# Kernel optimization log

Measured on AMD Instinct MI355X. Metric: run time of the kernel, lower is better.

## Reference

```python
import jax, jax.numpy as jnp
import numpy as np

B, T, C, H = 2, 2048, 1024, 16
N = C // H
MISS_ROWS = 128


def _rwkv7_scan(q, w_log, k, v, a, b):
    # all [B,T,H,N] float32 (bf16-rounded). RWKV7 delta-rule recurrence:
    #   S_t = S_{t-1} * diag(exp(w_t)) + (S_{t-1} a_t) b_t^T + v_t k_t^T
    #   o_t = S_t q_t   (state S has shape [B,H,Nv,Nk]; decay along k-dim)
    Bq, Tq, Hq, Nq = q.shape

    def step(S, inp):
        q_t, w_t, k_t, v_t, a_t, b_t = inp
        ew = jnp.exp(w_t)  # decay in (0,1) since w_log = -exp(...) < 0
        sa = jnp.einsum('bhvi,bhi->bhv', S, a_t)
        S = S * ew[:, :, None, :] + sa[..., None] * b_t[:, :, None, :] + v_t[..., None] * k_t[:, :, None, :]
        o = jnp.einsum('bhvj,bhj->bhv', S, q_t)
        return S, o

    xs = tuple(jnp.moveaxis(u, 1, 0) for u in (q, w_log, k, v, a, b))
    S0 = jnp.zeros((Bq, Hq, Nq, Nq), jnp.float32)
    _, o = jax.lax.scan(step, S0, xs)
    return jnp.moveaxis(o, 0, 1)  # [B,T,H,N]


def setup_inputs() -> dict:
    key = jax.random.key(0)
    ks = jax.random.split(key, 16)
    f32 = jnp.float32
    return {
        'residual': jax.random.normal(ks[0], (B, T, C), f32),
        'x': jax.random.normal(ks[1], (B, T, C), f32),
        'x0': jax.random.normal(ks[2], (B, T, C), f32),
        'dx0': jax.random.normal(ks[3], (B, T, C), f32),
        'Wq': jax.random.normal(ks[4], (C, C), f32) * 0.02,
        'Wk': jax.random.normal(ks[5], (C, C), f32) * 0.02,
        'Wv': jax.random.normal(ks[6], (C, C), f32) * 0.02,
        'Wproj': jax.random.normal(ks[7], (C, C), f32) * 0.02,
        'x_q': jax.random.uniform(ks[8], (1, 1, C), f32),
        'x_k': jax.random.uniform(ks[9], (1, 1, C), f32),
        'x_v': jax.random.uniform(ks[10], (1, 1, C), f32),
        'v0': 0.7 + 0.1 * jax.random.normal(ks[11], (1, 1, C), f32),
        'w0': -3.0 + 0.5 * jax.random.normal(ks[12], (1, 1, C), f32),
        'a0': 0.1 * jax.random.normal(ks[13], (1, 1, C), f32),
        'miss': jax.random.normal(ks[14], (MISS_ROWS, 4 * C), f32) * 0.02,
        'r_k': 0.1 * jax.random.normal(ks[15], (H, N), f32),
    }


def reference(residual, x, x0, dx0, Wq, Wk, Wv, Wproj, x_q, x_k, x_v, v0, w0, a0, miss, r_k):
    Bx, Tx, Cx = x.shape
    Hh, Nn = r_k.shape
    # token shift: dx_prev = x_{t-1} - x_t (zero-padded at t=0)
    dx_prev = jnp.concatenate([jnp.zeros_like(x[:, :1]), x[:, :-1]], axis=1) - x
    q = (x + dx_prev * x_q) @ Wq.T
    k = (x + dx_prev * x_k) @ Wk.T
    v = (x + dx_prev * x_v) @ Wv.T
    deltas = x[:, :, :miss.shape[0]] @ miss  # [B,T,4C]
    w_delta, v_delta, a_delta, g = jnp.split(deltas, 4, axis=-1)
    log_neglog_w = -jax.nn.softplus(-(w0 + w_delta)) - 0.5
    log_w = -jnp.exp(log_neglog_w)  # log decay, always < 0
    v_first = (x0 + dx0 * x_v) @ Wv.T
    v = v + (v_first - v) * jax.nn.sigmoid(v0 + v_delta)
    g = 1.0 + g
    a = jax.nn.sigmoid(a0 + a_delta)
    kh = k.reshape(Bx, Tx, Hh, Nn)
    kk = kh / jnp.maximum(jnp.linalg.norm(kh, axis=-1, keepdims=True), 1e-12)
    kk = kk.reshape(Bx, Tx, Cx)
    k = k * a
    z = -kk
    b = kk * a
    bf = lambda u: u.astype(jnp.bfloat16).astype(jnp.float32).reshape(Bx, Tx, Hh, Nn)
    qh, wh, kh2, vh, zh, bh = (bf(u) for u in (q, log_w, k, v, z, b))
    y = _rwkv7_scan(qh, wh, kh2, vh, zh, bh) * (float(Nn) ** -0.5)  # [B,T,H,N]
    xnorm = jnp.linalg.norm(x.reshape(Bx, Tx, Hh, Nn), axis=-1, keepdims=True)
    vnorm = jnp.linalg.norm(vh, axis=-1, keepdims=True)
    u = (1.0 - xnorm / (vnorm + 1e-12)) * jax.nn.sigmoid(r_k)
    y = (y + vh * u).reshape(Bx, Tx, Cx)
    y = y * g
    return residual + y @ Wproj.T
```

## Files before the change

### kernel.cpp

```cpp
#include <hip/hip_runtime.h>
#include <stdint.h>
#include <stddef.h>

#define B_ 2
#define T_ 2048
#define C_ 1024
#define H_ 16
#define N_ 64
#define M_ (B_*T_)
#define L_ 128
#define NC_ (T_/L_)

typedef unsigned short ushort_t;
typedef __attribute__((ext_vector_type(8))) __bf16 bf16x8;
typedef __attribute__((ext_vector_type(4))) float  f32x4;

__device__ __forceinline__ ushort_t f2bf(float x){
  uint32_t u = __float_as_uint(x);
  u += 0x7fffu + ((u >> 16) & 1u);
  return (ushort_t)(u >> 16);
}
__device__ __forceinline__ float bf2f(uint32_t hu){
  return __uint_as_float(hu << 16);
}
__device__ __forceinline__ void ldbf16x16(const ushort_t* p, float* o){
  uint4 u0 = *(const uint4*)p;
  uint4 u1 = *(const uint4*)(p+8);
  o[0]=bf2f(u0.x&0xffffu); o[1]=bf2f(u0.x>>16);
  o[2]=bf2f(u0.y&0xffffu); o[3]=bf2f(u0.y>>16);
  o[4]=bf2f(u0.z&0xffffu); o[5]=bf2f(u0.z>>16);
  o[6]=bf2f(u0.w&0xffffu); o[7]=bf2f(u0.w>>16);
  o[8]=bf2f(u1.x&0xffffu); o[9]=bf2f(u1.x>>16);
  o[10]=bf2f(u1.y&0xffffu); o[11]=bf2f(u1.y>>16);
  o[12]=bf2f(u1.z&0xffffu); o[13]=bf2f(u1.z>>16);
  o[14]=bf2f(u1.w&0xffffu); o[15]=bf2f(u1.w>>16);
}

__device__ __forceinline__ ushort4 mixq4(float4 a, float4 p, float4 c){
  ushort4 o;
  o.x = f2bf(fmaf(p.x - a.x, c.x, a.x));
  o.y = f2bf(fmaf(p.y - a.y, c.y, a.y));
  o.z = f2bf(fmaf(p.z - a.z, c.z, a.z));
  o.w = f2bf(fmaf(p.w - a.w, c.w, a.w));
  return o;
}
__global__ __launch_bounds__(256) void prep_all(
    const float* __restrict__ x, const float* __restrict__ x0,
    const float* __restrict__ dx0,
    const float* __restrict__ xq, const float* __restrict__ xk,
    const float* __restrict__ xv,
    const float* __restrict__ Wq, const float* __restrict__ Wk,
    const float* __restrict__ Wv, const float* __restrict__ Wp,
    const float* __restrict__ miss,
    ushort_t* __restrict__ Aq, ushort_t* __restrict__ Ak,
    ushort_t* __restrict__ Av, ushort_t* __restrict__ Axf,
    ushort_t* __restrict__ Xb,
    ushort_t* __restrict__ Wb, ushort_t* __restrict__ Wpb,
    ushort_t* __restrict__ missT)
{
  __shared__ ushort_t tile[128][66];
  const int blk = blockIdx.x;
  const int tid = threadIdx.x;
  if (blk < 4096){
    const int idx = blk*256 + tid;
    const int col4 = idx & 255;
    const int i = idx >> 8;
    const int t = i & (T_-1);
    float4 a = ((const float4*)x)[idx];
    float4 p = {0.f,0.f,0.f,0.f};
    if (t > 0) p = ((const float4*)x)[idx - 256];
    float4 cq = ((const float4*)xq)[col4];
    float4 ck = ((const float4*)xk)[col4];
    float4 cv = ((const float4*)xv)[col4];
    ((ushort4*)Aq)[idx] = mixq4(a, p, cq);
    ((ushort4*)Ak)[idx] = mixq4(a, p, ck);
    ((ushort4*)Av)[idx] = mixq4(a, p, cv);
    float4 z = ((const float4*)x0)[idx];
    float4 d = ((const float4*)dx0)[idx];
    ushort4 of;
    of.x = f2bf(fmaf(d.x, cv.x, z.x));
    of.y = f2bf(fmaf(d.y, cv.y, z.y));
    of.z = f2bf(fmaf(d.z, cv.z, z.z));
    of.w = f2bf(fmaf(d.w, cv.w, z.w));
    ((ushort4*)Axf)[idx] = of;
    ushort4 ob = {f2bf(a.x), f2bf(a.y), f2bf(a.z), f2bf(a.w)};
    ((ushort4*)Xb)[idx] = ob;
  } else if (blk < 4096 + 5*1024){
    const int y = (blk - 4096) >> 10;
    const float* src = (y==0)?Wq:(y==1)?Wk:(y<4)?Wv:Wp;
    ushort_t* dst = (y<4) ? Wb + (size_t)y*C_*C_ : Wpb;
    const int idx = ((blk - 4096) & 1023)*256 + tid;
    float4 v = ((const float4*)src)[idx];
    ushort4 o = {f2bf(v.x), f2bf(v.y), f2bf(v.z), f2bf(v.w)};
    ((ushort4*)dst)[idx] = o;
  } else {
    const int j0 = (blk - 4096 - 5*1024)*64;
#pragma unroll
    for (int rep=0; rep<8; rep++){
      int k = rep*16 + (tid>>4);
      int jj = (tid&15)*4;
      float4 v = *(const float4*)&miss[(size_t)k*4096 + j0 + jj];
      tile[k][jj+0]=f2bf(v.x); tile[k][jj+1]=f2bf(v.y);
      tile[k][jj+2]=f2bf(v.z); tile[k][jj+3]=f2bf(v.w);
    }
    __syncthreads();
#pragma unroll
    for (int rep=0; rep<8; rep++){
      int j = tid>>2;
      int kk = (tid&3)*32 + rep*4;
      ushort4 o = {tile[kk+0][j], tile[kk+1][j], tile[kk+2][j], tile[kk+3][j]};
      *(ushort4*)&missT[(size_t)(j0+j)*128 + kk] = o;
    }
  }
}

__global__ __launch_bounds__(256, 2) void mfma_gemm(
    const ushort_t* __restrict__ Ab, int lda, int64_t Asz,
    const ushort_t* __restrict__ Bbp, int ldb, int64_t Bsz,
    void* __restrict__ Cb, int ldc, int64_t Csz, int c_bf16,
    const float* __restrict__ resid, int K)
{
  const ushort_t* A  = Ab  + (size_t)blockIdx.z * Asz;
  const ushort_t* Bm = Bbp + (size_t)blockIdx.z * Bsz;
  const int i0 = blockIdx.y * 128;
  const int j0 = blockIdx.x * 128;
  const int tid = threadIdx.x;
  const int lane = tid & 63;
  const int w = tid >> 6;
  const int wm = w & 1, wn = w >> 1;

  __shared__ ushort_t As[128*32];
  __shared__ ushort_t Bs[128*32];

  f32x4 acc[4][4];
#pragma unroll
  for (int i=0;i<4;i++)
#pragma unroll
    for (int j=0;j<4;j++) acc[i][j] = (f32x4){0.f,0.f,0.f,0.f};

  const int lr = lane >> 2;
  const int ls = lane & 3;
  const ushort_t* ga = A  + (size_t)(i0 + w*32 + lr)*lda + ls*8;
  const ushort_t* gb = Bm + (size_t)(j0 + w*32 + lr)*ldb + ls*8;
  const int lm = lane & 15, lq = lane >> 4;

  for (int k0 = 0; k0 < K; k0 += 32){
    __syncthreads();
#pragma unroll
    for (int p=0;p<2;p++){
      __builtin_amdgcn_global_load_lds(
        (const __attribute__((address_space(1))) void*)(ga + (size_t)p*16*lda + k0),
        (__attribute__((address_space(3))) void*)&As[(w*32 + p*16)*32], 16, 0, 0);
      __builtin_amdgcn_global_load_lds(
        (const __attribute__((address_space(1))) void*)(gb + (size_t)p*16*ldb + k0),
        (__attribute__((address_space(3))) void*)&Bs[(w*32 + p*16)*32], 16, 0, 0);
    }
    __syncthreads();
    bf16x8 af[4], bfr[4];
#pragma unroll
    for (int i=0;i<4;i++)
      af[i] = *(const bf16x8*)&As[(wm*64 + i*16 + lm)*32 + lq*8];
#pragma unroll
    for (int j=0;j<4;j++)
      bfr[j] = *(const bf16x8*)&Bs[(wn*64 + j*16 + lm)*32 + lq*8];
#pragma unroll
    for (int i=0;i<4;i++)
#pragma unroll
      for (int j=0;j<4;j++)
        acc[i][j] = __builtin_amdgcn_mfma_f32_16x16x32_bf16(af[i], bfr[j], acc[i][j], 0, 0, 0);
  }

  if (!c_bf16){
    float* C = (float*)Cb + (size_t)blockIdx.z * Csz;
#pragma unroll
    for (int i=0;i<4;i++)
#pragma unroll
      for (int j=0;j<4;j++)
#pragma unroll
        for (int r=0;r<4;r++){
          const int row = i0 + wm*64 + i*16 + lq*4 + r;
          const int col = j0 + wn*64 + j*16 + lm;
          float v = acc[i][j][r];
          if (resid) v += resid[(size_t)row*ldc + col];
          C[(size_t)row*ldc + col] = v;
        }
  } else {
    ushort_t* C = (ushort_t*)Cb + (size_t)blockIdx.z * Csz;
#pragma unroll
    for (int i=0;i<4;i++)
#pragma unroll
      for (int j=0;j<4;j++)
#pragma unroll
        for (int r=0;r<4;r++){
          const int row = i0 + wm*64 + i*16 + lq*4 + r;
          const int col = j0 + wn*64 + j*16 + lm;
          C[(size_t)row*ldc + col] = f2bf(acc[i][j][r]);
        }
  }
}

__global__ __launch_bounds__(256) void fuse_kernel(
    const float* __restrict__ qm, const float* __restrict__ km,
    const float* __restrict__ vm, const float* __restrict__ vfm,
    const ushort_t* __restrict__ del, const float* __restrict__ x,
    const float* __restrict__ w0, const float* __restrict__ v0,
    const float* __restrict__ a0,
    uint32_t* __restrict__ packed, float* __restrict__ gout,
    float* __restrict__ ratio)
{
  const int lane = threadIdx.x & 63;
  const int ht = blockIdx.x*4 + (threadIdx.x >> 6);
  const int i = ht >> 4;
  const int h = ht & 15;
  const int c = h*64 + lane;
  const size_t ic = (size_t)i*C_ + c;
  float qv = qm[ic], kv = km[ic], vv = vm[ic], vfv = vfm[ic], xv = x[ic];
  const size_t d0 = (size_t)i*4*C_ + c;
  float wd = bf2f(del[d0]), vd = bf2f(del[d0+C_]);
  float ad = bf2f(del[d0+2*C_]), gd = bf2f(del[d0+3*C_]);

  float z1 = -(w0[c]+wd);
  float sp = fmaxf(z1, 0.f) + log1pf(expf(-fabsf(z1)));
  float logw = -expf(-sp - 0.5f);
  float sv = 1.f/(1.f+expf(-(v0[c]+vd)));
  vv = vv + (vfv - vv)*sv;
  float gv = 1.f + gd;
  float av = 1.f/(1.f+expf(-(a0[c]+ad)));

  ushort_t vr_u = f2bf(vv);
  float vrf = bf2f(vr_u);

  float ksq = kv*kv, xsq = xv*xv, vsq = vrf*vrf;
#pragma unroll
  for (int off=32; off>0; off>>=1){
    ksq += __shfl_xor(ksq, off, 64);
    xsq += __shfl_xor(xsq, off, 64);
    vsq += __shfl_xor(vsq, off, 64);
  }
  float kn = sqrtf(ksq);
  float kkn = kv / fmaxf(kn, 1e-12f);
  float k2 = kv*av;
  float zv = -kkn;
  float bv = kkn*av;

  uint32_t p0 = (uint32_t)f2bf(logw) | ((uint32_t)f2bf(zv) << 16);
  uint32_t p1 = (uint32_t)f2bf(bv)   | ((uint32_t)f2bf(k2) << 16);
  uint32_t p2 = (uint32_t)f2bf(qv)   | ((uint32_t)vr_u << 16);
  uint32_t* pb = packed + ((size_t)ht*64 + lane)*3;
  pb[0]=p0; pb[1]=p1; pb[2]=p2;
  gout[ic] = gv;
  if (lane == 0)
    ratio[ht] = 1.f - sqrtf(xsq)/(sqrtf(vsq)+1e-12f);
}


__global__ __launch_bounds__(256) void chunk_mdp_kernel(
    const uint32_t* __restrict__ packed,
    float* __restrict__ phi, float* __restrict__ cc, float* __restrict__ md)
{
  const int blk = blockIdx.x;
  const int c  = blk & (NC_-1);
  const int bh = blk >> 4;
  const int b = bh >> 4, h = bh & 15;
  const int tid = threadIdx.x;
  const int rp = tid >> 2;
  const int qr = tid & 3;
  const int t0 = c * L_;

  __shared__ float    ewS[4][N_], vS[4][N_];
  __shared__ ushort_t zS[4][N_], bS[4][N_], qS[4][N_], kS[4][N_];

  float X[16], Z[16];
#pragma unroll
  for (int i=0;i<16;i++){ X[i] = (qr*16+i == rp) ? 1.f : 0.f; Z[i] = 0.f; }

  const int s = tid >> 6, d = tid & 63;
  size_t ap = (((size_t)(b*T_+t0+s))*H_ + h)*64 + d;
  uint32_t pu0 = packed[ap*3], pu1 = packed[ap*3+1], pu2 = packed[ap*3+2];

  for (int tg = 0; tg < L_; tg += 4){
    __syncthreads();
    ewS[s][d] = __expf(bf2f(pu0 & 0xffffu));
    zS[s][d]  = (ushort_t)(pu0 >> 16);
    bS[s][d]  = (ushort_t)(pu1 & 0xffffu);
    kS[s][d]  = (ushort_t)(pu1 >> 16);
    qS[s][d]  = (ushort_t)(pu2 & 0xffffu);
    vS[s][d]  = bf2f(pu2 >> 16);
    if (tg + 4 < L_){
      size_t a2 = (((size_t)(b*T_+t0+tg+4+s))*H_ + h)*64 + d;
      pu0 = packed[a2*3]; pu1 = packed[a2*3+1]; pu2 = packed[a2*3+2];
    }
    __syncthreads();
#pragma unroll 1
    for (int ss=0; ss<4; ss++){
      float zf[16], ef[16], bf[16], qf[16], kf[16];
      ldbf16x16(&zS[ss][qr*16], zf);
      ldbf16x16(&bS[ss][qr*16], bf);
      ldbf16x16(&qS[ss][qr*16], qf);
      ldbf16x16(&kS[ss][qr*16], kf);
#pragma unroll
      for (int i4=0;i4<4;i4++)
        *(float4*)&ef[i4*4] = *(const float4*)&ewS[ss][qr*16+i4*4];
      const float vr = vS[ss][rp];
      float a0=0.f,a1=0.f,a2=0.f,a3=0.f, c0=0.f,c1=0.f,c2=0.f,c3=0.f;
#pragma unroll
      for (int i=0;i<16;i+=4){
        a0 = fmaf(X[i+0], zf[i+0], a0); a1 = fmaf(X[i+1], zf[i+1], a1);
        a2 = fmaf(X[i+2], zf[i+2], a2); a3 = fmaf(X[i+3], zf[i+3], a3);
        c0 = fmaf(Z[i+0], zf[i+0], c0); c1 = fmaf(Z[i+1], zf[i+1], c1);
        c2 = fmaf(Z[i+2], zf[i+2], c2); c3 = fmaf(Z[i+3], zf[i+3], c3);
      }
      float sx = (a0+a1)+(a2+a3);
      float sz = (c0+c1)+(c2+c3);
      sx += __shfl_xor(sx,1,64); sx += __shfl_xor(sx,2,64);
      sz += __shfl_xor(sz,1,64); sz += __shfl_xor(sz,2,64);
      float m0=0.f,m1=0.f,m2=0.f,m3=0.f, d0=0.f,d1=0.f,d2=0.f,d3=0.f;
#pragma unroll
      for (int i=0;i<16;i+=4){
        float t;
        t = fmaf(X[i+0], ef[i+0], sx*bf[i+0]); X[i+0]=t; m0 = fmaf(t, qf[i+0], m0);
        t = fmaf(X[i+1], ef[i+1], sx*bf[i+1]); X[i+1]=t; m1 = fmaf(t, qf[i+1], m1);
        t = fmaf(X[i+2], ef[i+2], sx*bf[i+2]); X[i+2]=t; m2 = fmaf(t, qf[i+2], m2);
        t = fmaf(X[i+3], ef[i+3], sx*bf[i+3]); X[i+3]=t; m3 = fmaf(t, qf[i+3], m3);
        t = fmaf(Z[i+0], ef[i+0], fmaf(sz, bf[i+0], vr*kf[i+0])); Z[i+0]=t; d0 = fmaf(t, qf[i+0], d0);
        t = fmaf(Z[i+1], ef[i+1], fmaf(sz, bf[i+1], vr*kf[i+1])); Z[i+1]=t; d1 = fmaf(t, qf[i+1], d1);
        t = fmaf(Z[i+2], ef[i+2], fmaf(sz, bf[i+2], vr*kf[i+2])); Z[i+2]=t; d2 = fmaf(t, qf[i+2], d2);
        t = fmaf(Z[i+3], ef[i+3], fmaf(sz, bf[i+3], vr*kf[i+3])); Z[i+3]=t; d3 = fmaf(t, qf[i+3], d3);
      }
      float mv = (m0+m1)+(m2+m3);
      float dv = (d0+d1)+(d2+d3);
      mv += __shfl_xor(mv,1,64); mv += __shfl_xor(mv,2,64);
      dv += __shfl_xor(dv,1,64); dv += __shfl_xor(dv,2,64);
      if (qr == 0)      md[((size_t)blk*L_ + tg+ss)*128 + rp]      = mv;
      else if (qr == 1) md[((size_t)blk*L_ + tg+ss)*128 + 64 + rp] = dv;
    }
  }
  const size_t base = (size_t)blk*4096 + (size_t)rp*64 + qr*16;
#pragma unroll
  for (int i4=0;i4<4;i4++){
    float4 xo = {X[i4*4+0],X[i4*4+1],X[i4*4+2],X[i4*4+3]};
    float4 zo = {Z[i4*4+0],Z[i4*4+1],Z[i4*4+2],Z[i4*4+3]};
    *(float4*)&phi[base + i4*4] = xo;
    *(float4*)&cc [base + i4*4] = zo;
  }
}

__global__ __launch_bounds__(256) void chunk_state_kernel(
    const float* __restrict__ phi, const float* __restrict__ cc,
    float* __restrict__ sstart)
{
  const int bh = blockIdx.x;
  const int tid = threadIdx.x;
  const int rb = tid >> 4;
  const int cq = tid & 15;
  __shared__ float Sld[64][65];
  __shared__ float Fld[64][68];
  float acc[4][4];
#pragma unroll
  for (int m=0;m<4;m++)
#pragma unroll
    for (int i=0;i<4;i++) acc[m][i] = 0.f;
#pragma unroll
  for (int m=0;m<4;m++){
    float4 z4 = {0.f,0.f,0.f,0.f};
    *(float4*)&Sld[rb+16*m][cq*4] = z4;
  }
  const float* pc = phi + (size_t)bh*NC_*4096;
  const float* cb = cc  + (size_t)bh*NC_*4096;
  float4 pf[4], pcc[4];
#pragma unroll
  for (int p=0;p<4;p++) pf[p] = *(const float4*)&pc[(size_t)p*1024 + tid*4];
#pragma unroll
  for (int m=0;m<4;m++) pcc[m] = *(const float4*)&cb[(size_t)(rb+16*m)*64 + cq*4];

  for (int c=0;c<NC_;c++){
    __syncthreads();
#pragma unroll
    for (int p=0;p<4;p++){
      int f = p*1024 + tid*4;
      *(float4*)&Fld[f>>6][f&63] = pf[p];
    }
    float na[4][4];
#pragma unroll
    for (int m=0;m<4;m++){
      na[m][0]=pcc[m].x; na[m][1]=pcc[m].y; na[m][2]=pcc[m].z; na[m][3]=pcc[m].w;
    }
#pragma unroll
    for (int m=0;m<4;m++){
      float4 so = {acc[m][0],acc[m][1],acc[m][2],acc[m][3]};
      *(float4*)&sstart[(size_t)(bh*NC_+c)*4096 + (size_t)(rb+16*m)*64 + cq*4] = so;
    }
    if (c+1 < NC_){
#pragma unroll
      for (int p=0;p<4;p++) pf[p] = *(const float4*)&pc[(size_t)(c+1)*4096 + p*1024 + tid*4];
#pragma unroll
      for (int m=0;m<4;m++) pcc[m] = *(const float4*)&cb[(size_t)(c+1)*4096 + (size_t)(rb+16*m)*64 + cq*4];
    }
    __syncthreads();
#pragma unroll 1
    for (int k0=0;k0<64;k0+=4){
      float4 sr[4];
#pragma unroll
      for (int m=0;m<4;m++) sr[m] = *(const float4*)&Sld[rb+16*m][k0];
      const float4 f0 = *(const float4*)&Fld[k0+0][cq*4];
      const float4 f1 = *(const float4*)&Fld[k0+1][cq*4];
      const float4 f2 = *(const float4*)&Fld[k0+2][cq*4];
      const float4 f3 = *(const float4*)&Fld[k0+3][cq*4];
#pragma unroll
      for (int m=0;m<4;m++){
        na[m][0] = fmaf(sr[m].x, f0.x, na[m][0]); na[m][0] = fmaf(sr[m].y, f1.x, na[m][0]);
        na[m][0] = fmaf(sr[m].z, f2.x, na[m][0]); na[m][0] = fmaf(sr[m].w, f3.x, na[m][0]);
        na[m][1] = fmaf(sr[m].x, f0.y, na[m][1]); na[m][1] = fmaf(sr[m].y, f1.y, na[m][1]);
        na[m][1] = fmaf(sr[m].z, f2.y, na[m][1]); na[m][1] = fmaf(sr[m].w, f3.y, na[m][1]);
        na[m][2] = fmaf(sr[m].x, f0.z, na[m][2]); na[m][2] = fmaf(sr[m].y, f1.z, na[m][2]);
        na[m][2] = fmaf(sr[m].z, f2.z, na[m][2]); na[m][2] = fmaf(sr[m].w, f3.z, na[m][2]);
        na[m][3] = fmaf(sr[m].x, f0.w, na[m][3]); na[m][3] = fmaf(sr[m].y, f1.w, na[m][3]);
        na[m][3] = fmaf(sr[m].z, f2.w, na[m][3]); na[m][3] = fmaf(sr[m].w, f3.w, na[m][3]);
      }
    }
    __syncthreads();
#pragma unroll
    for (int m=0;m<4;m++){
      float4 so = {na[m][0],na[m][1],na[m][2],na[m][3]};
      *(float4*)&Sld[rb+16*m][cq*4] = so;
#pragma unroll
      for (int i=0;i<4;i++) acc[m][i] = na[m][i];
    }
  }
}

__global__ __launch_bounds__(256) void chunk_emit_kernel(
    const uint32_t* __restrict__ packed, const float* __restrict__ ratio,
    const float* __restrict__ g, const float* __restrict__ rk,
    const float* __restrict__ sstart, const float* __restrict__ md,
    ushort_t* __restrict__ y)
{
  const int blk = blockIdx.x;
  const int c  = blk & (NC_-1);
  const int bh = blk >> 4;
  const int b = bh >> 4, h = bh & 15;
  const int tid = threadIdx.x;
  const int v = tid & 63;
  const int tg = tid >> 6;

  float4 sr[16];
  const float4* sp = (const float4*)(sstart + (size_t)blk*4096 + (size_t)v*64);
#pragma unroll
  for (int f=0;f<16;f++) sr[f] = sp[f];
  const float sigrk = 1.f/(1.f+__expf(-rk[h*64+v]));

#pragma unroll 1
  for (int ss=0; ss<32; ss++){
    const int t = tg*32 + ss;
    const int token = b*T_ + c*L_ + t;
    const float* mrow = md + ((size_t)blk*L_ + t)*128;
    float o0=0.f,o1=0.f,o2=0.f,o3=0.f;
#pragma unroll
    for (int f=0;f<16;f+=4){
      float4 m0 = ((const float4*)mrow)[f+0];
      float4 m1 = ((const float4*)mrow)[f+1];
      float4 m2 = ((const float4*)mrow)[f+2];
      float4 m3 = ((const float4*)mrow)[f+3];
      o0 = fmaf(sr[f+0].x,m0.x, fmaf(sr[f+0].y,m0.y, fmaf(sr[f+0].z,m0.z, fmaf(sr[f+0].w,m0.w, o0))));
      o1 = fmaf(sr[f+1].x,m1.x, fmaf(sr[f+1].y,m1.y, fmaf(sr[f+1].z,m1.z, fmaf(sr[f+1].w,m1.w, o1))));
      o2 = fmaf(sr[f+2].x,m2.x, fmaf(sr[f+2].y,m2.y, fmaf(sr[f+2].z,m2.z, fmaf(sr[f+2].w,m2.w, o2))));
      o3 = fmaf(sr[f+3].x,m3.x, fmaf(sr[f+3].y,m3.y, fmaf(sr[f+3].z,m3.z, fmaf(sr[f+3].w,m3.w, o3))));
    }
    float o = ((o0+o1)+(o2+o3)) + mrow[64 + v];
    const float vt = bf2f(packed[(((size_t)token*H_ + h)*64 + v)*3 + 2] >> 16);
    const float uv = ratio[(size_t)token*H_ + h];
    const float gv = g[(size_t)token*C_ + h*64 + v];
    y[(size_t)token*C_ + h*64 + v] = f2bf((o*0.125f + vt*uv*sigrk)*gv);
  }
}

extern "C" void kernel_launch(void* const* d_in, const int* in_sizes, int n_in,
                              void* d_out, int out_size, void* d_ws, size_t ws_size,
                              hipStream_t stream)
{
  const float* residual = (const float*)d_in[0];
  const float* x    = (const float*)d_in[1];
  const float* x0   = (const float*)d_in[2];
  const float* dx0  = (const float*)d_in[3];
  const float* Wq   = (const float*)d_in[4];
  const float* Wk   = (const float*)d_in[5];
  const float* Wv   = (const float*)d_in[6];
  const float* Wpr  = (const float*)d_in[7];
  const float* x_q  = (const float*)d_in[8];
  const float* x_k  = (const float*)d_in[9];
  const float* x_v  = (const float*)d_in[10];
  const float* v0   = (const float*)d_in[11];
  const float* w0   = (const float*)d_in[12];
  const float* a0   = (const float*)d_in[13];
  const float* miss = (const float*)d_in[14];
  const float* rk   = (const float*)d_in[15];
  float* out = (float*)d_out;

  char* ws = (char*)d_ws;
  const size_t MB = (size_t)1 << 20;
  float*    q_m    = (float*)(ws + 0*MB);
  float*    k_m    = (float*)(ws + 16*MB);
  float*    v_m    = (float*)(ws + 32*MB);
  float*    vf_m   = (float*)(ws + 48*MB);
  ushort_t* delb   = (ushort_t*)(ws + 64*MB);
  ushort_t* Ab     = (ushort_t*)(ws + 96*MB);
  ushort_t* Xb     = (ushort_t*)(ws + 128*MB);
  ushort_t* Wb     = (ushort_t*)(ws + 136*MB);
  uint32_t* packed = (uint32_t*)(ws + 96*MB);
  float*    g_m    = (float*)(ws + 144*MB);
  ushort_t* Wpb    = (ushort_t*)(ws + 160*MB);
  ushort_t* missT  = (ushort_t*)(ws + 162*MB);
  float*    ratio  = (float*)(ws + 163*MB);
  float*    phi    = (float*)(ws + 0*MB);
  float*    cc     = (float*)(ws + 16*MB);
  float*    sstart = (float*)(ws + 32*MB);
  ushort_t* yb     = (ushort_t*)(ws + 48*MB);
  float*    mdbuf  = (float*)(ws + 64*MB);

  ushort_t* Aq  = Ab + 0*(size_t)M_*C_;
  ushort_t* Ak  = Ab + 1*(size_t)M_*C_;
  ushort_t* Av  = Ab + 2*(size_t)M_*C_;
  ushort_t* Axf = Ab + 3*(size_t)M_*C_;

  dim3 blk(256);
  prep_all<<<4096 + 5*1024 + 64, blk, 0, stream>>>(
      x, x0, dx0, x_q, x_k, x_v, Wq, Wk, Wv, Wpr, miss,
      Aq, Ak, Av, Axf, Xb, Wb, Wpb, missT);
  mfma_gemm<<<dim3(C_/128, M_/128, 4), blk, 0, stream>>>(
      Ab, C_, (int64_t)M_*C_, Wb, C_, (int64_t)C_*C_,
      q_m, C_, (int64_t)M_*C_, 0, nullptr, C_);
  mfma_gemm<<<dim3(4*C_/128, M_/128, 1), blk, 0, stream>>>(
      Xb, C_, 0, missT, 128, 0, delb, 4*C_, 0, 1, nullptr, 128);
  fuse_kernel<<<M_*H_/4, blk, 0, stream>>>(q_m, k_m, v_m, vf_m, delb, x, w0, v0, a0, packed, g_m, ratio);
  chunk_mdp_kernel<<<B_*H_*NC_, blk, 0, stream>>>(packed, phi, cc, mdbuf);
  chunk_state_kernel<<<B_*H_, blk, 0, stream>>>(phi, cc, sstart);
  chunk_emit_kernel<<<B_*H_*NC_, blk, 0, stream>>>(packed, ratio, g_m, rk, sstart, mdbuf, yb);
  mfma_gemm<<<dim3(C_/128, M_/128, 1), blk, 0, stream>>>(
      yb, C_, 0, Wpb, C_, 0, out, C_, 0, 0, residual, C_);
}
```

Measured before the change: 548.0 us.

## Process two chunks per block in chunk_mdp with two rows per thread and DPP reductions

Each block of the chunk_mdp kernel now handles two chunks, with 128 threads per chunk, and each thread carries two state rows instead of one. This halves the grid and amortises the shared-memory loads of z, b, q, k and decay over two rows. The quad reductions switch from shfl_xor to DPP moves to cut cross-lane overhead. The cost is more registers per thread, fewer blocks (512 to 256) and less latency hiding on the serial scan.

```diff
diff --git a/kernel.cpp b/kernel.cpp
--- a/kernel.cpp
+++ b/kernel.cpp
@@ -34,6 +34,12 @@
   o[10]=bf2f(u1.y&0xffffu); o[11]=bf2f(u1.y>>16);
   o[12]=bf2f(u1.z&0xffffu); o[13]=bf2f(u1.z>>16);
   o[14]=bf2f(u1.w&0xffffu); o[15]=bf2f(u1.w>>16);
+}
+__device__ __forceinline__ float quad_sum(float v){
+  float a = __int_as_float(__builtin_amdgcn_mov_dpp(__float_as_int(v), 0xB1, 0xF, 0xF, true));
+  v += a;
+  float b = __int_as_float(__builtin_amdgcn_mov_dpp(__float_as_int(v), 0x4E, 0xF, 0xF, true));
+  return v + b;
 }
 
 __device__ __forceinline__ ushort4 mixq4(float4 a, float4 p, float4 c){
@@ -254,94 +260,117 @@
 }
 
 
-__global__ __launch_bounds__(256) void chunk_mdp_kernel(
+__global__ __launch_bounds__(256, 1) void chunk_mdp_kernel(
     const uint32_t* __restrict__ packed,
     float* __restrict__ phi, float* __restrict__ cc, float* __restrict__ md)
 {
-  const int blk = blockIdx.x;
-  const int c  = blk & (NC_-1);
-  const int bh = blk >> 4;
-  const int b = bh >> 4, h = bh & 15;
   const int tid = threadIdx.x;
-  const int rp = tid >> 2;
-  const int qr = tid & 3;
-  const int t0 = c * L_;
-
-  __shared__ float    ewS[4][N_], vS[4][N_];
-  __shared__ ushort_t zS[4][N_], bS[4][N_], qS[4][N_], kS[4][N_];
-
-  float X[16], Z[16];
-#pragma unroll
-  for (int i=0;i<16;i++){ X[i] = (qr*16+i == rp) ? 1.f : 0.f; Z[i] = 0.f; }
-
-  const int s = tid >> 6, d = tid & 63;
-  size_t ap = (((size_t)(b*T_+t0+s))*H_ + h)*64 + d;
-  uint32_t pu0 = packed[ap*3], pu1 = packed[ap*3+1], pu2 = packed[ap*3+2];
+  const int ch  = tid >> 7;
+  const int t7  = tid & 127;
+  const int rr  = t7 >> 2;
+  const int qr  = t7 & 3;
+
+  __shared__ float    ewS[2][4][N_], vS[2][4][N_];
+  __shared__ ushort_t zS[2][4][N_], bS[2][4][N_], qS[2][4][N_], kS[2][4][N_];
+
+  const int gcb = blockIdx.x*2;
+
+  uint32_t pu[2][3];
+#pragma unroll
+  for (int it=0; it<2; it++){
+    int slot = it*256 + tid;
+    int sc = slot >> 8, s = (slot >> 6) & 3, d = slot & 63;
+    int g = gcb + sc;
+    int cx = g & (NC_-1), bh = g >> 4;
+    int b = bh >> 4, h = bh & 15;
+    size_t ap = (((size_t)(b*T_ + cx*L_ + s))*H_ + h)*64 + d;
+    pu[it][0] = packed[ap*3]; pu[it][1] = packed[ap*3+1]; pu[it][2] = packed[ap*3+2];
+  }
+
+  float X0[16], X1[16], Z0[16], Z1[16];
+#pragma unroll
+  for (int i=0;i<16;i++){
+    X0[i] = (qr*16+i == 2*rr)   ? 1.f : 0.f;
+    X1[i] = (qr*16+i == 2*rr+1) ? 1.f : 0.f;
+    Z0[i] = 0.f; Z1[i] = 0.f;
+  }
 
   for (int tg = 0; tg < L_; tg += 4){
     __syncthreads();
-    ewS[s][d] = __expf(bf2f(pu0 & 0xffffu));
-    zS[s][d]  = (ushort_t)(pu0 >> 16);
-    bS[s][d]  = (ushort_t)(pu1 & 0xffffu);
-    kS[s][d]  = (ushort_t)(pu1 >> 16);
-    qS[s][d]  = (ushort_t)(pu2 & 0xffffu);
-    vS[s][d]  = bf2f(pu2 >> 16);
+#pragma unroll
+    for (int it=0; it<2; it++){
+      int slot = it*256 + tid;
+      int sc = slot >> 8, s = (slot >> 6) & 3, d = slot & 63;
+      ewS[sc][s][d] = __expf(bf2f(pu[it][0] & 0xffffu));
+      zS[sc][s][d]  = (ushort_t)(pu[it][0] >> 16);
+      bS[sc][s][d]  = (ushort_t)(pu[it][1] & 0xffffu);
+      kS[sc][s][d]  = (ushort_t)(pu[it][1] >> 16);
+      qS[sc][s][d]  = (ushort_t)(pu[it][2] & 0xffffu);
+      vS[sc][s][d]  = bf2f(pu[it][2] >> 16);
+    }
     if (tg + 4 < L_){
-      size_t a2 = (((size_t)(b*T_+t0+tg+4+s))*H_ + h)*64 + d;
-      pu0 = packed[a2*3]; pu1 = packed[a2*3+1]; pu2 = packed[a2*3+2];
+#pragma unroll
+      for (int it=0; it<2; it++){
+        int slot = it*256 + tid;
+        int sc = slot >> 8, s = (slot >> 6) & 3, d = slot & 63;
+        int g = gcb + sc;
+        int cx = g & (NC_-1), bh = g >> 4;
+        int b = bh >> 4, h = bh & 15;
+        size_t ap = (((size_t)(b*T_ + cx*L_ + tg+4+s))*H_ + h)*64 + d;
+        pu[it][0] = packed[ap*3]; pu[it][1] = packed[ap*3+1]; pu[it][2] = packed[ap*3+2];
+      }
     }
     __syncthreads();
 #pragma unroll 1
     for (int ss=0; ss<4; ss++){
-      float zf[16], ef[16], bf[16], qf[16], kf[16];
-      ldbf16x16(&zS[ss][qr*16], zf);
-      ldbf16x16(&bS[ss][qr*16], bf);
-      ldbf16x16(&qS[ss][qr*16], qf);
-      ldbf16x16(&kS[ss][qr*16], kf);
+      float zf[16];
+      ldbf16x16(&zS[ch][ss][qr*16], zf);
+      float sx0=0.f, sx1=0.f, sz0=0.f, sz1=0.f;
+#pragma unroll
+      for (int i=0;i<16;i++){
+        sx0 = fmaf(X0[i], zf[i], sx0);
+        sx1 = fmaf(X1[i], zf[i], sx1);
+        sz0 = fmaf(Z0[i], zf[i], sz0);
+        sz1 = fmaf(Z1[i], zf[i], sz1);
+      }
+      sx0 = quad_sum(sx0); sx1 = quad_sum(sx1);
+      sz0 = quad_sum(sz0); sz1 = quad_sum(sz1);
+
+      float ef[16], bf[16], qf[16], kf[16];
 #pragma unroll
       for (int i4=0;i4<4;i4++)
-        *(float4*)&ef[i4*4] = *(const float4*)&ewS[ss][qr*16+i4*4];
-      const float vr = vS[ss][rp];
-      float a0=0.f,a1=0.f,a2=0.f,a3=0.f, c0=0.f,c1=0.f,c2=0.f,c3=0.f;
-#pragma unroll
-      for (int i=0;i<16;i+=4){
-        a0 = fmaf(X[i+0], zf[i+0], a0); a1 = fmaf(X[i+1], zf[i+1], a1);
-        a2 = fmaf(X[i+2], zf[i+2], a2); a3 = fmaf(X[i+3], zf[i+3], a3);
-        c0 = fmaf(Z[i+0], zf[i+0], c0); c1 = fmaf(Z[i+1], zf[i+1], c1);
-        c2 = fmaf(Z[i+2], zf[i+2], c2); c3 = fmaf(Z[i+3], zf[i+3], c3);
+        *(float4*)&ef[i4*4] = *(const float4*)&ewS[ch][ss][qr*16+i4*4];
+      ldbf16x16(&bS[ch][ss][qr*16], bf);
+      ldbf16x16(&qS[ch][ss][qr*16], qf);
+      ldbf16x16(&kS[ch][ss][qr*16], kf);
+      const float v0r = vS[ch][ss][2*rr];
+      const float v1r = vS[ch][ss][2*rr+1];
+
+      float m0=0.f,m1=0.f,d0=0.f,d1=0.f;
+#pragma unroll
+      for (int i=0;i<16;i++){
+        float t;
+        t = fmaf(X0[i], ef[i], sx0*bf[i]); X0[i]=t; m0 = fmaf(t, qf[i], m0);
+        t = fmaf(X1[i], ef[i], sx1*bf[i]); X1[i]=t; m1 = fmaf(t, qf[i], m1);
+        t = fmaf(Z0[i], ef[i], fmaf(sz0, bf[i], v0r*kf[i])); Z0[i]=t; d0 = fmaf(t, qf[i], d0);
+        t = fmaf(Z1[i], ef[i], fmaf(sz1, bf[i], v1r*kf[i])); Z1[i]=t; d1 = fmaf(t, qf[i], d1);
       }
-      float sx = (a0+a1)+(a2+a3);
-      float sz = (c0+c1)+(c2+c3);
-      sx += __shfl_xor(sx,1,64); sx += __shfl_xor(sx,2,64);
-      sz += __shfl_xor(sz,1,64); sz += __shfl_xor(sz,2,64);
-      float m0=0.f,m1=0.f,m2=0.f,m3=0.f, d0=0.f,d1=0.f,d2=0.f,d3=0.f;
-#pragma unroll
-      for (int i=0;i<16;i+=4){
-        float t;
-        t = fmaf(X[i+0], ef[i+0], sx*bf[i+0]); X[i+0]=t; m0 = fmaf(t, qf[i+0], m0);
-        t = fmaf(X[i+1], ef[i+1], sx*bf[i+1]); X[i+1]=t; m1 = fmaf(t, qf[i+1], m1);
-        t = fmaf(X[i+2], ef[i+2], sx*bf[i+2]); X[i+2]=t; m2 = fmaf(t, qf[i+2], m2);
-        t = fmaf(X[i+3], ef[i+3], sx*bf[i+3]); X[i+3]=t; m3 = fmaf(t, qf[i+3], m3);
-        t = fmaf(Z[i+0], ef[i+0], fmaf(sz, bf[i+0], vr*kf[i+0])); Z[i+0]=t; d0 = fmaf(t, qf[i+0], d0);
-        t = fmaf(Z[i+1], ef[i+1], fmaf(sz, bf[i+1], vr*kf[i+1])); Z[i+1]=t; d1 = fmaf(t, qf[i+1], d1);
-        t = fmaf(Z[i+2], ef[i+2], fmaf(sz, bf[i+2], vr*kf[i+2])); Z[i+2]=t; d2 = fmaf(t, qf[i+2], d2);
-        t = fmaf(Z[i+3], ef[i+3], fmaf(sz, bf[i+3], vr*kf[i+3])); Z[i+3]=t; d3 = fmaf(t, qf[i+3], d3);
-      }
-      float mv = (m0+m1)+(m2+m3);
-      float dv = (d0+d1)+(d2+d3);
-      mv += __shfl_xor(mv,1,64); mv += __shfl_xor(mv,2,64);
-      dv += __shfl_xor(dv,1,64); dv += __shfl_xor(dv,2,64);
-      if (qr == 0)      md[((size_t)blk*L_ + tg+ss)*128 + rp]      = mv;
-      else if (qr == 1) md[((size_t)blk*L_ + tg+ss)*128 + 64 + rp] = dv;
-    }
-  }
-  const size_t base = (size_t)blk*4096 + (size_t)rp*64 + qr*16;
+      m0 = quad_sum(m0); m1 = quad_sum(m1);
+      d0 = quad_sum(d0); d1 = quad_sum(d1);
+      const size_t mb = ((size_t)(gcb+ch)*L_ + tg+ss)*128;
+      if      (qr == 0) md[mb + 2*rr]      = m0;
+      else if (qr == 1) md[mb + 2*rr+1]    = m1;
+      else if (qr == 2) md[mb + 64 + 2*rr]   = d0;
+      else              md[mb + 64 + 2*rr+1] = d1;
+    }
+  }
+  const size_t base = (size_t)(gcb+ch)*4096 + (size_t)(2*rr)*64 + qr*16;
 #pragma unroll
   for (int i4=0;i4<4;i4++){
-    float4 xo = {X[i4*4+0],X[i4*4+1],X[i4*4+2],X[i4*4+3]};
-    float4 zo = {Z[i4*4+0],Z[i4*4+1],Z[i4*4+2],Z[i4*4+3]};
-    *(float4*)&phi[base + i4*4] = xo;
-    *(float4*)&cc [base + i4*4] = zo;
+    *(float4*)&phi[base + i4*4]      = (float4){X0[i4*4+0],X0[i4*4+1],X0[i4*4+2],X0[i4*4+3]};
+    *(float4*)&phi[base + 64 + i4*4] = (float4){X1[i4*4+0],X1[i4*4+1],X1[i4*4+2],X1[i4*4+3]};
+    *(float4*)&cc [base + i4*4]      = (float4){Z0[i4*4+0],Z0[i4*4+1],Z0[i4*4+2],Z0[i4*4+3]};
+    *(float4*)&cc [base + 64 + i4*4] = (float4){Z1[i4*4+0],Z1[i4*4+1],Z1[i4*4+2],Z1[i4*4+3]};
   }
 }
 
@@ -532,7 +561,7 @@
   mfma_gemm<<<dim3(4*C_/128, M_/128, 1), blk, 0, stream>>>(
       Xb, C_, 0, missT, 128, 0, delb, 4*C_, 0, 1, nullptr, 128);
   fuse_kernel<<<M_*H_/4, blk, 0, stream>>>(q_m, k_m, v_m, vf_m, delb, x, w0, v0, a0, packed, g_m, ratio);
-  chunk_mdp_kernel<<<B_*H_*NC_, blk, 0, stream>>>(packed, phi, cc, mdbuf);
+  chunk_mdp_kernel<<<B_*H_*NC_/2, blk, 0, stream>>>(packed, phi, cc, mdbuf);
   chunk_state_kernel<<<B_*H_, blk, 0, stream>>>(phi, cc, sstart);
   chunk_emit_kernel<<<B_*H_*NC_, blk, 0, stream>>>(packed, ratio, g_m, rk, sstart, mdbuf, yb);
   mfma_gemm<<<dim3(C_/128, M_/128, 1), blk, 0, stream>>>(
```

Measured after the change: 529.8 us. 1.03x faster.
